# Kernel tuning notes

Measured on AMD Instinct MI355X. Metric: run time of the kernel, lower is better.

## Reference

```python
import jax, jax.numpy as jnp
import numpy as np


def setup_inputs() -> dict:
    key = jax.random.key(0)
    k1, k2 = jax.random.split(key)
    x = jax.random.normal(k1, (8, 18, 64, 64), dtype=jnp.float32)
    sp = jax.random.normal(k2, (4096, 18), dtype=jnp.float32)
    sp = sp / jnp.linalg.norm(sp, axis=-1, keepdims=True)  # unit-norm codebook
    return {"x": x, "super_points": sp}


def reference(x, super_points):
    # x: [b, d, h, w]; super_points: [K, d], unit norm.
    b, d, h, w = x.shape
    xt = jnp.transpose(x, (0, 2, 3, 1)).reshape(b, h * w, d)  # b n d
    xn = xt / jnp.linalg.norm(xt, axis=-1, keepdims=True)      # on-sphere
    # Both xn and codebook are unit norm, so argmin of L2 distance over the
    # codebook == argmax of cosine similarity; compute the N x K sims once.
    sims = jnp.einsum('bnd,kd->bnk', xn, super_points)         # b n K
    indices = jnp.argmax(sims, axis=-1)                        # b n
    quantized = super_points[indices]                          # b n d (gather)
    # entropy regularizer (training path)
    logits = sims * 100.0
    log_probs = jax.nn.log_softmax(logits + 1e-15, axis=-1)
    probs = jnp.exp(log_probs)
    sample_entropy = -jnp.sum(probs * log_probs, axis=-1)      # b n
    avg_probs = jnp.mean(probs, axis=(0, 1))                   # K
    entro_mean = jnp.mean(sample_entropy)
    mean_entro = -jnp.sum(avg_probs * jnp.log(avg_probs + 1e-15))
    entro_loss = entro_mean - mean_entro
    # straight-through estimator + commitment loss
    q_ste = xn + jax.lax.stop_gradient(quantized - xn)
    commit_loss = jnp.mean((xn - jax.lax.stop_gradient(q_ste)) ** 2)
    q = jnp.transpose(q_ste.reshape(b, h, w, d), (0, 3, 1, 2))  # b d h w
    return q, indices.reshape(-1), entro_mean, mean_entro, entro_loss, commit_loss
```

## Files before the change

kernel.cpp:

```cpp
#include <hip/hip_runtime.h>
#include <hip/hip_bf16.h>
#include <math.h>

#define D       18
#define KCB     4096
#define NROW    32768
#define RPB     64
#define NWAVE   8
#define KTPW    32
#define NBLK    (NROW / RPB)

#define P100     144.26950408889634f
#define SEED1    (-152.26950408889634f)
#define LN2f     0.6931471805599453f
#define INVP100  0.006931471805599453f
#define DELTA    0.25f

#define Q_OFF   0
#define IDX_OFF 589824
#define SCL_OFF 622592

#define WS_SCAL  0
#define WS_KVEC  16
#define WS_SPEXT 8192
#define WS_PART  139264
#define WS_END   (WS_PART + NBLK * KCB)

typedef __attribute__((ext_vector_type(8))) short bf16x8;
typedef __attribute__((ext_vector_type(4))) float f32x4;

__device__ __forceinline__ unsigned int f2bf(float f, float& residual)
{
    __hip_bfloat16 b = __float2bfloat16(f);
    residual = f - __bfloat162float(b);
    union { __hip_bfloat16 b; unsigned short u; } cv;
    cv.b = b;
    return (unsigned int)cv.u;
}

__global__ __launch_bounds__(256)
void hs_prep(const float* __restrict__ sp, unsigned int* __restrict__ spx)
{
    const int k  = blockIdx.x * 256 + threadIdx.x;
    const int kt = k >> 4, r = k & 15;
    unsigned int hu[18], lu[18];
#pragma unroll
    for (int j = 0; j < D; ++j) {
        float res, res2;
        hu[j] = f2bf(sp[k * D + j], res);
        lu[j] = f2bf(res, res2);
    }
    unsigned int w[32];
#pragma unroll
    for (int i = 0; i < 9; ++i) {
        unsigned int hwv = hu[2 * i] | (hu[2 * i + 1] << 16);
        unsigned int lwv = lu[2 * i] | (lu[2 * i + 1] << 16);
        w[i] = hwv; w[9 + i] = hwv; w[18 + i] = lwv;
    }
#pragma unroll
    for (int i = 27; i < 32; ++i) w[i] = 0;
#pragma unroll
    for (int g = 0; g < 4; ++g) {
        unsigned int* dst = spx + (size_t)kt * 512 + (g * 16 + r) * 8;
        *(uint4*)(dst)     = make_uint4(w[g*4], w[g*4+1], w[g*4+2], w[g*4+3]);
        *(uint4*)(dst + 4) = make_uint4(w[16+g*4], w[16+g*4+1], w[16+g*4+2], w[16+g*4+3]);
    }
}

__global__ __launch_bounds__(512, 4)
void hs_main(const float* __restrict__ x, const float* __restrict__ sp,
             float* __restrict__ out_q, float* __restrict__ out_idx,
             float* __restrict__ ws_scal, const unsigned int* __restrict__ spx,
             float* __restrict__ ws_part, float* __restrict__ ws_kvec)
{
    __shared__ unsigned int xe[RPB][36];
    __shared__ float        xsl_lds[RPB][20];
    __shared__ float        zw[NWAVE][RPB];
    __shared__ unsigned int k1w[NWAVE][RPB], k2w[NWAVE][RPB];
    __shared__ float        An_lds[RPB];
    __shared__ float        entw[NWAVE];

    const int tid = threadIdx.x;
    const int l   = tid & 63;
    const int wu  = __builtin_amdgcn_readfirstlane(tid >> 6);
    const int col = l & 15, g = l >> 4;
    const int row = blockIdx.x * RPB + l;
    const int b   = row >> 12;
    const int p   = row & 4095;

    if (wu == 0) {
        float xs[D];
        float ssq = 0.f;
#pragma unroll
        for (int j = 0; j < D; ++j) {
            float v = x[(b * D + j) * 4096 + p];
            xs[j] = v;
            ssq += v * v;
        }
        const float sf = (1.0f / sqrtf(ssq)) * P100;
#pragma unroll
        for (int j = 0; j < D; ++j) xs[j] *= sf;
#pragma unroll
        for (int j = 0; j < D; ++j) xsl_lds[l][j] = xs[j];

        unsigned int hu[18], lu[18];
#pragma unroll
        for (int j = 0; j < D; ++j) {
            float res, res2;
            hu[j] = f2bf(xs[j], res);
            lu[j] = f2bf(res, res2);
        }
#pragma unroll
        for (int i = 0; i < 9; ++i) {
            unsigned int hwv = hu[2 * i] | (hu[2 * i + 1] << 16);
            unsigned int lwv = lu[2 * i] | (lu[2 * i + 1] << 16);
            xe[l][i] = hwv; xe[l][9 + i] = lwv; xe[l][18 + i] = hwv;
        }
#pragma unroll
        for (int i = 27; i < 32; ++i) xe[l][i] = 0;
    }
    __syncthreads();

    union { uint4 u; bf16x8 v; } cv;
    bf16x8 fxlo[4], fxhi[4];
#pragma unroll
    for (int pt = 0; pt < 4; ++pt) {
        cv.u = *(const uint4*)&xe[pt * 16 + col][g * 4];      fxlo[pt] = cv.v;
        cv.u = *(const uint4*)&xe[pt * 16 + col][16 + g * 4]; fxhi[pt] = cv.v;
    }

    float Zp[4] = {0.f, 0.f, 0.f, 0.f};
    unsigned int k1p[4] = {0u, 0u, 0u, 0u};
    unsigned int k2p[4] = {0u, 0u, 0u, 0u};
    const int kof = g * 4;
    const int kt0 = wu * KTPW;

#pragma unroll 2
    for (int kt = 0; kt < KTPW; ++kt) {
        const uint4* ap = (const uint4*)(spx + (size_t)(kt0 + kt) * 512 + l * 8);
        cv.u = ap[0]; const bf16x8 alo = cv.v;
        cv.u = ap[1]; const bf16x8 ahi = cv.v;
        const unsigned int inv0 = 4095u - (unsigned int)((kt0 + kt) * 16 + kof);
#pragma unroll
        for (int pt = 0; pt < 4; ++pt) {
            f32x4 c = {SEED1, SEED1, SEED1, SEED1};
            c = __builtin_amdgcn_mfma_f32_16x16x32_bf16(alo, fxlo[pt], c, 0, 0, 0);
            c = __builtin_amdgcn_mfma_f32_16x16x32_bf16(ahi, fxhi[pt], c, 0, 0, 0);
#pragma unroll
            for (int r = 0; r < 4; ++r) {
                const float t = c[r];
                const unsigned int okey = ~__float_as_uint(t);
                const unsigned int key = (okey & 0xFFFFF000u) | (inv0 - (unsigned)r);
                k2p[pt] = max(k2p[pt], min(k1p[pt], key));
                k1p[pt] = max(k1p[pt], key);
                Zp[pt] += __builtin_amdgcn_exp2f(t);
            }
        }
    }

#pragma unroll
    for (int off = 16; off < 64; off <<= 1) {
#pragma unroll
        for (int pt = 0; pt < 4; ++pt) {
            Zp[pt] += __shfl_xor(Zp[pt], off);
            unsigned int ok1 = (unsigned int)__shfl_xor((int)k1p[pt], off);
            unsigned int ok2 = (unsigned int)__shfl_xor((int)k2p[pt], off);
            k2p[pt] = max(max(k2p[pt], ok2), min(k1p[pt], ok1));
            k1p[pt] = max(k1p[pt], ok1);
        }
    }
    if (g == 0) {
#pragma unroll
        for (int pt = 0; pt < 4; ++pt) {
            const int px = pt * 16 + col;
            zw[wu][px] = Zp[pt];
            k1w[wu][px] = k1p[pt];
            k2w[wu][px] = k2p[pt];
        }
    }
    __syncthreads();

    if (wu == 0) {
        float Zt = zw[0][l];
        unsigned int k1 = k1w[0][l], k2 = k2w[0][l];
#pragma unroll
        for (int s = 1; s < NWAVE; ++s) {
            Zt += zw[s][l];
            unsigned int ok1 = k1w[s][l], ok2 = k2w[s][l];
            k2 = max(max(k2, ok2), min(k1, ok1));
            k1 = max(k1, ok1);
        }
        const float l2Z = log2f(Zt);
        An_lds[l] = -(P100 + 8.0f + l2Z);

        float xsl[D];
#pragma unroll
        for (int j = 0; j < D; ++j) xsl[j] = xsl_lds[l][j];

        int i1 = 4095 - (int)(k1 & 0xFFFu);
        int i2 = 4095 - (int)(k2 & 0xFFFu);
        const float tq1 = __uint_as_float(~(k1 | 0xFFFu));
        const float tq2 = __uint_as_float(~(k2 | 0xFFFu));
        int it = i1;
        if (tq1 - tq2 < DELTA) {
            const float2* r1 = (const float2*)(sp + i1 * D);
            const float2* r2 = (const float2*)(sp + i2 * D);
            float d1 = 0.f, d2 = 0.f;
#pragma unroll
            for (int j = 0; j < 9; ++j) {
                d1 = fmaf(xsl[2 * j], r1[j].x, d1);
                d1 = fmaf(xsl[2 * j + 1], r1[j].y, d1);
                d2 = fmaf(xsl[2 * j], r2[j].x, d2);
                d2 = fmaf(xsl[2 * j + 1], r2[j].y, d2);
            }
            if (d2 > d1 || (d2 == d1 && i2 < i1)) it = i2;
        }
        out_idx[row] = (float)it;

        float2 gq[9];
        const float2* gr = (const float2*)(sp + it * D);
#pragma unroll
        for (int j = 0; j < 9; ++j) gq[j] = gr[j];
        float cp = 0.f;
#pragma unroll
        for (int j = 0; j < 9; ++j) {
            float qx = gq[j].x, qy = gq[j].y;
            float dx = fmaf(xsl[2 * j],     INVP100, -qx);
            float dy = fmaf(xsl[2 * j + 1], INVP100, -qy);
            cp = fmaf(dx, dx, cp);
            cp = fmaf(dy, dy, cp);
            out_q[(b * D + 2 * j)     * 4096 + p] = qx;
            out_q[(b * D + 2 * j + 1) * 4096 + p] = qy;
        }

        float v2 = cp;
#pragma unroll
        for (int off = 1; off < 64; off <<= 1) v2 += __shfl_xor(v2, off);
        if (l == 0) atomicAdd(&ws_scal[1], v2);
    }
    __syncthreads();

    float4 an4[4];
#pragma unroll
    for (int pt = 0; pt < 4; ++pt)
        an4[pt] = *(const float4*)&An_lds[pt * 16 + kof];

    float entacc = 0.f;
    float* pdst = ws_part ? ws_part + (size_t)blockIdx.x * KCB : nullptr;
#pragma unroll 2
    for (int kt = 0; kt < KTPW; ++kt) {
        const uint4* ap = (const uint4*)(spx + (size_t)(kt0 + kt) * 512 + l * 8);
        cv.u = ap[0]; const bf16x8 alo = cv.v;
        cv.u = ap[1]; const bf16x8 ahi = cv.v;

        float ksum = 0.f;
#pragma unroll
        for (int pt = 0; pt < 4; ++pt) {
            f32x4 c = {an4[pt].x, an4[pt].y, an4[pt].z, an4[pt].w};
            c = __builtin_amdgcn_mfma_f32_16x16x32_bf16(fxlo[pt], alo, c, 0, 0, 0);
            c = __builtin_amdgcn_mfma_f32_16x16x32_bf16(fxhi[pt], ahi, c, 0, 0, 0);
#pragma unroll
            for (int r = 0; r < 4; ++r) {
                const float t2 = c[r];
                const float e = __builtin_amdgcn_exp2f(t2);
                ksum += e;
                entacc = fmaf(e, t2, entacc);
            }
        }
        ksum += __shfl_xor(ksum, 16);
        ksum += __shfl_xor(ksum, 32);
        if (g == 0) {
            const int kk = (kt0 + kt) * 16 + col;
            if (pdst) pdst[kk] = ksum;
            else      atomicAdd(&ws_kvec[kk], ksum);
        }
    }

#pragma unroll
    for (int off = 1; off < 64; off <<= 1) entacc += __shfl_xor(entacc, off);
    if (l == 0) entw[wu] = entacc;
    __syncthreads();
    if (tid == 0) {
        float e = 0.f;
#pragma unroll
        for (int s = 0; s < NWAVE; ++s) e += entw[s];
        atomicAdd(&ws_scal[0], e);
    }
}

__global__ void hs_reduce(const float* __restrict__ part, float* __restrict__ kvec)
{
    const int kb = blockIdx.x & 15;
    const int sb = blockIdx.x >> 4;
    const int k  = kb * 256 + threadIdx.x;
    const float* pp = part + (size_t)sb * 32 * KCB + k;
    float s = 0.f;
#pragma unroll 8
    for (int bb = 0; bb < 32; ++bb) s += pp[bb * KCB];
    atomicAdd(&kvec[k], s);
}

__global__ void hs_final(const float* __restrict__ ws_kvec,
                         const float* __restrict__ ws_scal,
                         float* __restrict__ out)
{
    __shared__ float red[4];
    const int tid = threadIdx.x;
    float local = 0.f;
    for (int k = tid; k < KCB; k += 256) {
        float a = ws_kvec[k] * (1.0f / 32768.0f);
        local += a * (log2f(a + 1e-15f) * LN2f);
    }
#pragma unroll
    for (int off = 1; off < 64; off <<= 1) local += __shfl_xor(local, off);
    if ((tid & 63) == 0) red[tid >> 6] = local;
    __syncthreads();
    if (tid == 0) {
        float mean_entro = -(red[0] + red[1] + red[2] + red[3]);
        float entro_mean = -LN2f * ws_scal[0] * (1.0f / 32768.0f);
        float commit     = ws_scal[1] * (1.0f / (32768.0f * 18.0f));
        out[SCL_OFF + 0] = entro_mean;
        out[SCL_OFF + 1] = mean_entro;
        out[SCL_OFF + 2] = entro_mean - mean_entro;
        out[SCL_OFF + 3] = commit;
    }
}

extern "C" void kernel_launch(void* const* d_in, const int* in_sizes, int n_in,
                              void* d_out, int out_size, void* d_ws, size_t ws_size,
                              hipStream_t stream)
{
    const float* x  = (const float*)d_in[0];
    const float* sp = (const float*)d_in[1];
    float* out = (float*)d_out;
    float* ws  = (float*)d_ws;

    const bool partials = ws_size >= (size_t)WS_END * sizeof(float);

    hipMemsetAsync(ws, 0, (WS_KVEC + KCB) * sizeof(float), stream);

    hs_prep<<<16, 256, 0, stream>>>(sp, (unsigned int*)(ws + WS_SPEXT));
    hs_main<<<NBLK, 512, 0, stream>>>(x, sp, out + Q_OFF, out + IDX_OFF,
                                      ws + WS_SCAL,
                                      (const unsigned int*)(ws + WS_SPEXT),
                                      partials ? ws + WS_PART : nullptr,
                                      ws + WS_KVEC);
    if (partials)
        hs_reduce<<<256, 256, 0, stream>>>(ws + WS_PART, ws + WS_KVEC);
    hs_final<<<1, 256, 0, stream>>>(ws + WS_KVEC, ws + WS_SCAL, out);
}
```

Baseline: 81.10 us.

## Halve rows per block, defer argmin/gather tail, accumulate paired partials atomically

Each block now handles 32 rows with two MFMA point tiles instead of 64 rows with four, which doubles the grid and raises the launch-bounds occupancy target. The serial wave-0 phase (argmin refinement, gather, output writes, commitment loss) moves after the entropy pass, removing one barrier stage. The log-normaliser is now computed per lane and spread with shuffles instead of going through LDS. Argmax keys use a min-based encoding with no bit inversion. Block pairs atomically add into 512 partial rows, which requires an extra workspace memset and doubles codebook loads per unit of MFMA work.

```diff
diff --git a/kernel.cpp b/kernel.cpp
--- a/kernel.cpp
+++ b/kernel.cpp
@@ -5,10 +5,12 @@
 #define D       18
 #define KCB     4096
 #define NROW    32768
-#define RPB     64
+#define RPB     32
+#define NPT     2
 #define NWAVE   8
 #define KTPW    32
 #define NBLK    (NROW / RPB)
+#define NPART   512
 
 #define P100     144.26950408889634f
 #define SEED1    (-152.26950408889634f)
@@ -24,7 +26,7 @@
 #define WS_KVEC  16
 #define WS_SPEXT 8192
 #define WS_PART  139264
-#define WS_END   (WS_PART + NBLK * KCB)
+#define WS_END   (WS_PART + NPART * KCB)
 
 typedef __attribute__((ext_vector_type(8))) short bf16x8;
 typedef __attribute__((ext_vector_type(4))) float f32x4;
@@ -67,7 +69,7 @@
     }
 }
 
-__global__ __launch_bounds__(512, 4)
+__global__ __launch_bounds__(512, 8)
 void hs_main(const float* __restrict__ x, const float* __restrict__ sp,
              float* __restrict__ out_q, float* __restrict__ out_idx,
              float* __restrict__ ws_scal, const unsigned int* __restrict__ spx,
@@ -77,18 +79,18 @@
     __shared__ float        xsl_lds[RPB][20];
     __shared__ float        zw[NWAVE][RPB];
     __shared__ unsigned int k1w[NWAVE][RPB], k2w[NWAVE][RPB];
-    __shared__ float        An_lds[RPB];
     __shared__ float        entw[NWAVE];
 
     const int tid = threadIdx.x;
     const int l   = tid & 63;
     const int wu  = __builtin_amdgcn_readfirstlane(tid >> 6);
     const int col = l & 15, g = l >> 4;
-    const int row = blockIdx.x * RPB + l;
+    const int kof = g * 4;
+    const int row = blockIdx.x * RPB + (l & 31);
     const int b   = row >> 12;
     const int p   = row & 4095;
 
-    if (wu == 0) {
+    if (wu == 0 && l < 32) {
         float xs[D];
         float ssq = 0.f;
 #pragma unroll
@@ -122,17 +124,17 @@
     __syncthreads();
 
     union { uint4 u; bf16x8 v; } cv;
-    bf16x8 fxlo[4], fxhi[4];
-#pragma unroll
-    for (int pt = 0; pt < 4; ++pt) {
+    bf16x8 fxlo[NPT], fxhi[NPT];
+#pragma unroll
+    for (int pt = 0; pt < NPT; ++pt) {
         cv.u = *(const uint4*)&xe[pt * 16 + col][g * 4];      fxlo[pt] = cv.v;
         cv.u = *(const uint4*)&xe[pt * 16 + col][16 + g * 4]; fxhi[pt] = cv.v;
     }
 
-    float Zp[4] = {0.f, 0.f, 0.f, 0.f};
-    unsigned int k1p[4] = {0u, 0u, 0u, 0u};
-    unsigned int k2p[4] = {0u, 0u, 0u, 0u};
-    const int kof = g * 4;
+    float Zp[NPT] = {0.f, 0.f};
+    unsigned int k1p[NPT] = {0xFFFFFFFFu, 0xFFFFFFFFu};
+    unsigned int k2p[NPT] = {0xFFFFFFFFu, 0xFFFFFFFFu};
+    const unsigned int MASKV = 0xFFFFF000u;
     const int kt0 = wu * KTPW;
 
 #pragma unroll 2
@@ -140,19 +142,19 @@
         const uint4* ap = (const uint4*)(spx + (size_t)(kt0 + kt) * 512 + l * 8);
         cv.u = ap[0]; const bf16x8 alo = cv.v;
         cv.u = ap[1]; const bf16x8 ahi = cv.v;
-        const unsigned int inv0 = 4095u - (unsigned int)((kt0 + kt) * 16 + kof);
-#pragma unroll
-        for (int pt = 0; pt < 4; ++pt) {
+        const unsigned int kb = (unsigned int)(((kt0 + kt) << 4) + kof);
+#pragma unroll
+        for (int pt = 0; pt < NPT; ++pt) {
             f32x4 c = {SEED1, SEED1, SEED1, SEED1};
             c = __builtin_amdgcn_mfma_f32_16x16x32_bf16(alo, fxlo[pt], c, 0, 0, 0);
             c = __builtin_amdgcn_mfma_f32_16x16x32_bf16(ahi, fxhi[pt], c, 0, 0, 0);
 #pragma unroll
             for (int r = 0; r < 4; ++r) {
                 const float t = c[r];
-                const unsigned int okey = ~__float_as_uint(t);
-                const unsigned int key = (okey & 0xFFFFF000u) | (inv0 - (unsigned)r);
-                k2p[pt] = max(k2p[pt], min(k1p[pt], key));
-                k1p[pt] = max(k1p[pt], key);
+                const unsigned int key =
+                    (__float_as_uint(t) & MASKV) | (kb + (unsigned)r);
+                k2p[pt] = min(k2p[pt], max(k1p[pt], key));
+                k1p[pt] = min(k1p[pt], key);
                 Zp[pt] += __builtin_amdgcn_exp2f(t);
             }
         }
@@ -161,17 +163,17 @@
 #pragma unroll
     for (int off = 16; off < 64; off <<= 1) {
 #pragma unroll
-        for (int pt = 0; pt < 4; ++pt) {
+        for (int pt = 0; pt < NPT; ++pt) {
             Zp[pt] += __shfl_xor(Zp[pt], off);
             unsigned int ok1 = (unsigned int)__shfl_xor((int)k1p[pt], off);
             unsigned int ok2 = (unsigned int)__shfl_xor((int)k2p[pt], off);
-            k2p[pt] = max(max(k2p[pt], ok2), min(k1p[pt], ok1));
-            k1p[pt] = max(k1p[pt], ok1);
+            k2p[pt] = min(min(k2p[pt], ok2), max(k1p[pt], ok1));
+            k1p[pt] = min(k1p[pt], ok1);
         }
     }
     if (g == 0) {
 #pragma unroll
-        for (int pt = 0; pt < 4; ++pt) {
+        for (int pt = 0; pt < NPT; ++pt) {
             const int px = pt * 16 + col;
             zw[wu][px] = Zp[pt];
             k1w[wu][px] = k1p[pt];
@@ -180,73 +182,19 @@
     }
     __syncthreads();
 
-    if (wu == 0) {
-        float Zt = zw[0][l];
-        unsigned int k1 = k1w[0][l], k2 = k2w[0][l];
-#pragma unroll
-        for (int s = 1; s < NWAVE; ++s) {
-            Zt += zw[s][l];
-            unsigned int ok1 = k1w[s][l], ok2 = k2w[s][l];
-            k2 = max(max(k2, ok2), min(k1, ok1));
-            k1 = max(k1, ok1);
-        }
-        const float l2Z = log2f(Zt);
-        An_lds[l] = -(P100 + 8.0f + l2Z);
-
-        float xsl[D];
-#pragma unroll
-        for (int j = 0; j < D; ++j) xsl[j] = xsl_lds[l][j];
-
-        int i1 = 4095 - (int)(k1 & 0xFFFu);
-        int i2 = 4095 - (int)(k2 & 0xFFFu);
-        const float tq1 = __uint_as_float(~(k1 | 0xFFFu));
-        const float tq2 = __uint_as_float(~(k2 | 0xFFFu));
-        int it = i1;
-        if (tq1 - tq2 < DELTA) {
-            const float2* r1 = (const float2*)(sp + i1 * D);
-            const float2* r2 = (const float2*)(sp + i2 * D);
-            float d1 = 0.f, d2 = 0.f;
-#pragma unroll
-            for (int j = 0; j < 9; ++j) {
-                d1 = fmaf(xsl[2 * j], r1[j].x, d1);
-                d1 = fmaf(xsl[2 * j + 1], r1[j].y, d1);
-                d2 = fmaf(xsl[2 * j], r2[j].x, d2);
-                d2 = fmaf(xsl[2 * j + 1], r2[j].y, d2);
-            }
-            if (d2 > d1 || (d2 == d1 && i2 < i1)) it = i2;
-        }
-        out_idx[row] = (float)it;
-
-        float2 gq[9];
-        const float2* gr = (const float2*)(sp + it * D);
-#pragma unroll
-        for (int j = 0; j < 9; ++j) gq[j] = gr[j];
-        float cp = 0.f;
-#pragma unroll
-        for (int j = 0; j < 9; ++j) {
-            float qx = gq[j].x, qy = gq[j].y;
-            float dx = fmaf(xsl[2 * j],     INVP100, -qx);
-            float dy = fmaf(xsl[2 * j + 1], INVP100, -qy);
-            cp = fmaf(dx, dx, cp);
-            cp = fmaf(dy, dy, cp);
-            out_q[(b * D + 2 * j)     * 4096 + p] = qx;
-            out_q[(b * D + 2 * j + 1) * 4096 + p] = qy;
-        }
-
-        float v2 = cp;
-#pragma unroll
-        for (int off = 1; off < 64; off <<= 1) v2 += __shfl_xor(v2, off);
-        if (l == 0) atomicAdd(&ws_scal[1], v2);
-    }
-    __syncthreads();
-
-    float4 an4[4];
-#pragma unroll
-    for (int pt = 0; pt < 4; ++pt)
-        an4[pt] = *(const float4*)&An_lds[pt * 16 + kof];
+    float Zt = 0.f;
+#pragma unroll
+    for (int s = 0; s < NWAVE; ++s) Zt += zw[s][l & 31];
+    const float Anl = -(P100 + 8.0f + __builtin_amdgcn_logf(Zt));
+    float an[NPT][4];
+#pragma unroll
+    for (int pt = 0; pt < NPT; ++pt)
+#pragma unroll
+        for (int r = 0; r < 4; ++r)
+            an[pt][r] = __shfl(Anl, pt * 16 + kof + r);
 
     float entacc = 0.f;
-    float* pdst = ws_part ? ws_part + (size_t)blockIdx.x * KCB : nullptr;
+    float* pdst = ws_part ? ws_part + (size_t)(blockIdx.x >> 1) * KCB : nullptr;
 #pragma unroll 2
     for (int kt = 0; kt < KTPW; ++kt) {
         const uint4* ap = (const uint4*)(spx + (size_t)(kt0 + kt) * 512 + l * 8);
@@ -255,8 +203,8 @@
 
         float ksum = 0.f;
 #pragma unroll
-        for (int pt = 0; pt < 4; ++pt) {
-            f32x4 c = {an4[pt].x, an4[pt].y, an4[pt].z, an4[pt].w};
+        for (int pt = 0; pt < NPT; ++pt) {
+            f32x4 c = {an[pt][0], an[pt][1], an[pt][2], an[pt][3]};
             c = __builtin_amdgcn_mfma_f32_16x16x32_bf16(fxlo[pt], alo, c, 0, 0, 0);
             c = __builtin_amdgcn_mfma_f32_16x16x32_bf16(fxhi[pt], ahi, c, 0, 0, 0);
 #pragma unroll
@@ -271,7 +219,7 @@
         ksum += __shfl_xor(ksum, 32);
         if (g == 0) {
             const int kk = (kt0 + kt) * 16 + col;
-            if (pdst) pdst[kk] = ksum;
+            if (pdst) atomicAdd(pdst + kk, ksum);
             else      atomicAdd(&ws_kvec[kk], ksum);
         }
     }
@@ -285,6 +233,60 @@
 #pragma unroll
         for (int s = 0; s < NWAVE; ++s) e += entw[s];
         atomicAdd(&ws_scal[0], e);
+    }
+
+    if (wu == 0) {
+        float cp = 0.f;
+        if (l < 32) {
+            unsigned int k1 = 0xFFFFFFFFu, k2 = 0xFFFFFFFFu;
+#pragma unroll
+            for (int s = 0; s < NWAVE; ++s) {
+                unsigned int ok1 = k1w[s][l], ok2 = k2w[s][l];
+                k2 = min(min(k2, ok2), max(k1, ok1));
+                k1 = min(k1, ok1);
+            }
+            float xsl[D];
+#pragma unroll
+            for (int j = 0; j < D; ++j) xsl[j] = xsl_lds[l][j];
+
+            int i1 = (int)(k1 & 0xFFFu);
+            int i2 = (int)(k2 & 0xFFFu);
+            const float tq1 = __uint_as_float(k1 & 0xFFFFF000u);
+            const float tq2 = __uint_as_float(k2 & 0xFFFFF000u);
+            int it = i1;
+            if (tq1 - tq2 < DELTA) {
+                const float2* r1 = (const float2*)(sp + i1 * D);
+                const float2* r2 = (const float2*)(sp + i2 * D);
+                float d1 = 0.f, d2 = 0.f;
+#pragma unroll
+                for (int j = 0; j < 9; ++j) {
+                    d1 = fmaf(xsl[2 * j], r1[j].x, d1);
+                    d1 = fmaf(xsl[2 * j + 1], r1[j].y, d1);
+                    d2 = fmaf(xsl[2 * j], r2[j].x, d2);
+                    d2 = fmaf(xsl[2 * j + 1], r2[j].y, d2);
+                }
+                if (d2 > d1 || (d2 == d1 && i2 < i1)) it = i2;
+            }
+            out_idx[row] = (float)it;
+
+            float2 gq[9];
+            const float2* gr = (const float2*)(sp + it * D);
+#pragma unroll
+            for (int j = 0; j < 9; ++j) gq[j] = gr[j];
+#pragma unroll
+            for (int j = 0; j < 9; ++j) {
+                float qx = gq[j].x, qy = gq[j].y;
+                float dx = fmaf(xsl[2 * j],     INVP100, -qx);
+                float dy = fmaf(xsl[2 * j + 1], INVP100, -qy);
+                cp = fmaf(dx, dx, cp);
+                cp = fmaf(dy, dy, cp);
+                out_q[(b * D + 2 * j)     * 4096 + p] = qx;
+                out_q[(b * D + 2 * j + 1) * 4096 + p] = qy;
+            }
+#pragma unroll
+            for (int off = 1; off < 32; off <<= 1) cp += __shfl_xor(cp, off);
+            if (l == 0) atomicAdd(&ws_scal[1], cp);
+        }
     }
 }
 
@@ -338,6 +340,8 @@
     const bool partials = ws_size >= (size_t)WS_END * sizeof(float);
 
     hipMemsetAsync(ws, 0, (WS_KVEC + KCB) * sizeof(float), stream);
+    if (partials)
+        hipMemsetAsync(ws + WS_PART, 0, (size_t)NPART * KCB * sizeof(float), stream);
 
     hs_prep<<<16, 256, 0, stream>>>(sp, (unsigned int*)(ws + WS_SPEXT));
     hs_main<<<NBLK, 512, 0, stream>>>(x, sp, out + Q_OFF, out + IDX_OFF,
```

After: 143.5 us. 76.9% more time.
